# Optimization experiments

Measured on AMD Instinct MI355X. Metric: run time of the kernel, lower is better.

## Reference

```python
import jax, jax.numpy as jnp
import numpy as np

B, C, H, W = 512, 1, 128, 128
RS, WS = 12, 12
L, HID, T = 128, 512, 16


def setup_inputs() -> dict:
    key = jax.random.key(0)
    ks = jax.random.split(key, 24)

    def u(k, shape, fan):
        return jax.random.uniform(k, shape, jnp.float32, -1.0, 1.0) / np.sqrt(fan)

    enc_in = 2 * RS * RS + HID  # 800
    inp = {
        "x": jax.random.uniform(ks[0], (B, C, H, W), jnp.float32),
        "eps": jax.random.normal(ks[1], (T, B, L), jnp.float32),
        "glimpses": T,
        "canvas_init": jnp.zeros((C, H, W), jnp.float32),
        "h_dec_init": jnp.zeros((HID,), jnp.float32),
        "h_enc_init": jnp.zeros((HID,), jnp.float32),
        "W_ih_enc": u(ks[2], (4 * HID, enc_in), enc_in),
        "b_ih_enc": u(ks[3], (4 * HID,), enc_in),
        "W_hh_enc": u(ks[4], (4 * HID, HID), HID),
        "b_hh_enc": u(ks[5], (4 * HID,), HID),
        "W_ih_dec": u(ks[6], (4 * HID, L), L),
        "b_ih_dec": u(ks[7], (4 * HID,), L),
        "W_hh_dec": u(ks[8], (4 * HID, HID), HID),
        "b_hh_dec": u(ks[9], (4 * HID,), HID),
        "W_samp": u(ks[10], (2 * L, HID), HID),
        "b_samp": u(ks[11], (2 * L,), HID),
        "W_rattn": u(ks[12], (5, HID), HID),
        "b_rattn": u(ks[13], (5,), HID),
        "W_wattn": u(ks[14], (5, HID), HID),
        "b_wattn": u(ks[15], (5,), HID),
        "W_writer": u(ks[16], (WS * WS, HID), HID),
        "b_writer": u(ks[17], (WS * WS,), HID),
    }
    return inp


def _lstm_cell(x, h, c, Wih, bih, Whh, bhh):
    gates = x @ Wih.T + bih + h @ Whh.T + bhh
    i, f, g, o = jnp.split(gates, 4, axis=-1)
    c_new = jax.nn.sigmoid(f) * c + jax.nn.sigmoid(i) * jnp.tanh(g)
    h_new = jax.nn.sigmoid(o) * jnp.tanh(c_new)
    return h_new, c_new


def _filter_bank(gx, gy, variance, stride, size):
    # gx, gy, variance, stride: [B,1]
    offsets = (jnp.arange(size, dtype=jnp.float32) + 0.5 - size / 2) * stride  # [B,size]
    mu_x = (gx + offsets)[..., None]  # [B,size,1]
    mu_y = (gy + offsets)[..., None]
    var = variance[:, :, None]  # [B,1,1]
    a = jnp.arange(W, dtype=jnp.float32)
    b = jnp.arange(H, dtype=jnp.float32)
    Fx = jnp.exp(-((a - mu_x) ** 2) / (2 * var))  # [B,size,W]
    Fy = jnp.exp(-((b - mu_y) ** 2) / (2 * var))  # [B,size,H]
    Fx = Fx / jnp.maximum(Fx.sum(axis=2, keepdims=True), 1e-8)
    Fy = Fy / jnp.maximum(Fy.sum(axis=2, keepdims=True), 1e-8)
    return Fx, Fy


def _attn_window(h_state, Wattn, battn, size):
    res = h_state @ Wattn.T + battn  # [B,5]
    gx_, gy_, log_var, log_delta, log_inten = [res[:, i:i + 1] for i in range(5)]
    gx = (W + 1) * (gx_ + 1) / 2
    gy = (H + 1) * (gy_ + 1) / 2
    stride = (max(H, W) - 1) * jnp.exp(log_delta) / (size - 1)
    Fx, Fy = _filter_bank(gx, gy, jnp.exp(log_var), stride, size)
    return Fx, Fy, jnp.exp(log_inten)


def _read(x, x_error, h_dec, W_rattn, b_rattn):
    Fx, Fy, inten = _attn_window(h_dec, W_rattn, b_rattn, RS)
    FxT = jnp.swapaxes(Fx, -1, -2)[:, None]  # [B,1,W,RS]
    Fy = Fy[:, None]  # [B,1,RS,H]
    glimpse = jnp.concatenate((Fy @ x @ FxT, Fy @ x_error @ FxT), axis=1)  # [B,2C,RS,RS]
    return inten[:, :, None, None] * glimpse


def _write(h_dec, W_writer, b_writer, W_wattn, b_wattn):
    w = (h_dec @ W_writer.T + b_writer).reshape(-1, C, WS, WS)
    Fx, Fy, inten = _attn_window(h_dec, W_wattn, b_wattn, WS)
    FyT = jnp.swapaxes(Fy, -1, -2)[:, None]  # [B,1,H,WS]
    Fx = Fx[:, None]  # [B,1,WS,W]
    return (FyT @ w @ Fx) / inten[:, :, None, None]  # [B,C,H,W]


def reference(x, eps, glimpses, canvas_init, h_dec_init, h_enc_init,
              W_ih_enc, b_ih_enc, W_hh_enc, b_hh_enc,
              W_ih_dec, b_ih_dec, W_hh_dec, b_hh_dec,
              W_samp, b_samp, W_rattn, b_rattn, W_wattn, b_wattn,
              W_writer, b_writer):
    batch = x.shape[0]
    canvas0 = jnp.broadcast_to(canvas_init, (batch, C, H, W))
    h_dec0 = jnp.broadcast_to(h_dec_init, (batch, HID))
    h_enc0 = jnp.broadcast_to(h_enc_init, (batch, HID))
    c0 = jnp.zeros((batch, HID), x.dtype)

    def step(carry, eps_t):
        canvas, h_enc, c_enc, h_dec, c_dec = carry
        x_error = x - jax.nn.sigmoid(canvas)
        r = _read(x, x_error, h_dec, W_rattn, b_rattn).reshape(batch, -1)
        enc_in = jnp.concatenate((r, h_dec), axis=1)
        h_enc, c_enc = _lstm_cell(enc_in, h_enc, c_enc, W_ih_enc, b_ih_enc, W_hh_enc, b_hh_enc)
        s = h_enc @ W_samp.T + b_samp
        mu, log_var = s[:, :L], s[:, L:]
        z = mu + jnp.exp(log_var * 0.5) * eps_t
        h_dec, c_dec = _lstm_cell(z, h_dec, c_dec, W_ih_dec, b_ih_dec, W_hh_dec, b_hh_dec)
        canvas = canvas + _write(h_dec, W_writer, b_writer, W_wattn, b_wattn)
        return (canvas, h_enc, c_enc, h_dec, c_dec), (mu, log_var)

    (canvas, _, _, _, _), (mus, log_vars) = jax.lax.scan(
        step, (canvas0, h_enc0, c0, h_dec0, c0), eps[:glimpses])
    # mus/log_vars: [T,B,L] -> [B,T,L] to match torch.stack(mu, dim=1)
    return jax.nn.sigmoid(canvas), jnp.swapaxes(mus, 0, 1), jnp.swapaxes(log_vars, 0, 1)
```

## Files before the change

kernel.cpp:

```cpp
#include <hip/hip_runtime.h>
#include <hip/hip_bf16.h>
#include <math.h>

#define BATCH 512
#define HID 512
#define LAT 128
#define TSTEPS 16
#define IMG 16384
#define ENC_IN 800
#define GATES 2048

#define SEC_E 1344
#define SEC_D 640

typedef __attribute__((ext_vector_type(8))) short short8;
typedef __attribute__((ext_vector_type(4))) float f32x4;

__device__ __forceinline__ void gload16(const void* g, void* l) {
    __builtin_amdgcn_global_load_lds((const __attribute__((address_space(1))) unsigned int*)g,
                                     (__attribute__((address_space(3))) unsigned int*)l, 16, 0, 0);
}

__device__ __forceinline__ void bsplit(float v, unsigned short& hi, unsigned short& lo) {
    unsigned u = __float_as_uint(v);
    unsigned uh = (u + (0x7FFFu + ((u >> 16) & 1u))) & 0xFFFF0000u;
    hi = (unsigned short)(uh >> 16);
    float r = v - __uint_as_float(uh);
    unsigned ur = __float_as_uint(r);
    unsigned ul = (ur + (0x7FFFu + ((ur >> 16) & 1u))) & 0xFFFF0000u;
    lo = (unsigned short)(ul >> 16);
}

__global__ __launch_bounds__(256) void init_canvas(float* __restrict__ canvas,
                                                   const float* __restrict__ ci) {
    int idx = blockIdx.x * 256 + threadIdx.x;
    canvas[idx] = ci[idx & (IMG - 1)];
}

__global__ __launch_bounds__(256) void init_state(float* __restrict__ he, float* __restrict__ ce,
                                                  float* __restrict__ hd, float* __restrict__ cd,
                                                  const float* __restrict__ hei,
                                                  const float* __restrict__ hdi,
                                                  unsigned short* __restrict__ A_enc,
                                                  unsigned short* __restrict__ A_dec) {
    int idx = blockIdx.x * 256 + threadIdx.x;
    int b = idx >> 9, u = idx & 511;
    float ve = hei[u], vd = hdi[u];
    he[idx] = ve;
    hd[idx] = vd;
    ce[idx] = 0.f;
    cd[idx] = 0.f;
    unsigned short hi, lo;
    bsplit(ve, hi, lo);
    size_t be = (size_t)b * 2 * SEC_E;
    A_enc[be + 800 + u] = hi;
    A_enc[be + SEC_E + 800 + u] = lo;
    bsplit(vd, hi, lo);
    size_t bd = (size_t)b * 2 * SEC_D;
    A_dec[bd + 128 + u] = hi;
    A_dec[bd + SEC_D + 128 + u] = lo;
}

__global__ __launch_bounds__(256) void sigmoid_final(float* __restrict__ c) {
    int idx = blockIdx.x * 256 + threadIdx.x;
    c[idx] = 1.f / (1.f + expf(-c[idx]));
}

__global__ __launch_bounds__(256) void prep_wsplit(const float* __restrict__ W1, int K1,
                                                   const float* __restrict__ W2, int K2,
                                                   unsigned short* __restrict__ out, int SEC) {
    int kk = blockIdx.x * 256 + threadIdx.x;
    int n = blockIdx.y;
    if (kk >= SEC) return;
    float v = 0.f;
    if (kk < K1) v = W1[(size_t)n * K1 + kk];
    else if (kk < K1 + K2) v = W2[(size_t)n * K2 + (kk - K1)];
    unsigned short hi, lo;
    bsplit(v, hi, lo);
    size_t base = (size_t)n * 2 * SEC;
    out[base + kk] = hi;
    out[base + SEC + kk] = lo;
}

__global__ __launch_bounds__(256) void gemm_bf16x3(const unsigned short* __restrict__ Au,
                                                   const unsigned short* __restrict__ Wu,
                                                   float* __restrict__ C, int SEC,
                                                   int ktb0, int kte0, int ktb1, int kte1) {
    __shared__ __align__(16) char lds[2][16384];
    const __bf16* A = (const __bf16*)Au;
    const __bf16* Wt = (const __bf16*)Wu;
    const int ld = 2 * SEC;
    const int tid = threadIdx.x;
    const int z = blockIdx.z;
    const int bm = blockIdx.x * 64;
    const int bn = blockIdx.y * 64;
    const int ktb = z ? ktb1 : ktb0;
    const int kte = z ? kte1 : kte0;

    const int row0 = tid >> 3, c0 = tid & 7;
    const size_t ga0 = (size_t)(bm + row0) * ld + (size_t)((c0 ^ (row0 & 7)) * 8);
    const size_t ga1 = ga0 + (size_t)32 * ld;
    const size_t gb0 = (size_t)(bn + row0) * ld + (size_t)((c0 ^ (row0 & 7)) * 8);
    const size_t gb1 = gb0 + (size_t)32 * ld;
    const int lA0 = tid * 16, lA1 = (tid + 256) * 16;
    const int lB0 = 8192 + tid * 16, lB1 = 8192 + (tid + 256) * 16;

    const int lane = tid & 63, wv = tid >> 6;
    const int rA = wv * 16 + (lane & 15);
    const int chnk = (lane >> 4) ^ (lane & 7);
    const int byteA = rA * 128 + chnk * 16;
    const int byteB = 8192 + (lane & 15) * 128 + chnk * 16;

    f32x4 acc[4];
#pragma unroll
    for (int j = 0; j < 4; ++j) acc[j] = (f32x4){0.f, 0.f, 0.f, 0.f};

    auto STAGE = [&](int buf, int kt) {
        const int kw = kt * 64;
        const int ka = (kw >= SEC) ? (kw - SEC) : kw;
        const int kb = (kw >= 2 * SEC) ? (kw - 2 * SEC) : kw;
        const __bf16* a = A + ka;
        const __bf16* w = Wt + kb;
        char* l = &lds[buf][0];
        gload16(a + ga0, l + lA0);
        gload16(a + ga1, l + lA1);
        gload16(w + gb0, l + lB0);
        gload16(w + gb1, l + lB1);
    };

    STAGE(0, ktb);
    asm volatile("s_waitcnt vmcnt(0)" ::: "memory");
    __syncthreads();
    int buf = 0;
    for (int kt = ktb; kt < kte; ++kt) {
        if (kt + 1 < kte) STAGE(buf ^ 1, kt + 1);
        const char* base = &lds[buf][0];
        short8 a0 = *(const short8*)(base + byteA);
        short8 a1 = *(const short8*)(base + (byteA ^ 64));
#pragma unroll
        for (int j = 0; j < 4; ++j) {
            short8 b0 = *(const short8*)(base + (byteB + j * 2048));
            short8 b1 = *(const short8*)(base + ((byteB + j * 2048) ^ 64));
            acc[j] = __builtin_amdgcn_mfma_f32_16x16x32_bf16(a0, b0, acc[j], 0, 0, 0);
            acc[j] = __builtin_amdgcn_mfma_f32_16x16x32_bf16(a1, b1, acc[j], 0, 0, 0);
        }
        asm volatile("s_waitcnt vmcnt(0)" ::: "memory");
        __syncthreads();
        buf ^= 1;
    }
    float* Cz = C + (size_t)z * BATCH * GATES;
    const int crow = bm + wv * 16 + (lane >> 4) * 4;
    const int ccol = bn + (lane & 15);
#pragma unroll
    for (int j = 0; j < 4; ++j)
#pragma unroll
        for (int r = 0; r < 4; ++r)
            Cz[(size_t)(crow + r) * GATES + ccol + j * 16] = acc[j][r];
}

__global__ __launch_bounds__(256) void read_glimpse_fused(const float* __restrict__ x,
                                                          const float* __restrict__ canvas,
                                                          const float* __restrict__ h_dec,
                                                          const float* __restrict__ Wa,
                                                          const float* __restrict__ ba,
                                                          unsigned short* __restrict__ A_enc) {
    const int b = blockIdx.x, t = threadIdx.x;
    __shared__ float red[5][256];
    __shared__ float par[5];
    __shared__ float fx[12][132], fy[12][132];
    __shared__ float dnx[12], dny[12];
    __shared__ float pbuf[4][12][128];
    __shared__ float tm[12][132], te[12][132];
    const float* hb = h_dec + (size_t)b * HID;
#pragma unroll
    for (int j = 0; j < 5; ++j)
        red[j][t] = hb[t] * Wa[j * HID + t] + hb[t + 256] * Wa[j * HID + t + 256];
    __syncthreads();
    for (int o = 128; o > 0; o >>= 1) {
        if (t < o) {
#pragma unroll
            for (int j = 0; j < 5; ++j) red[j][t] += red[j][t + o];
        }
        __syncthreads();
    }
    if (t < 5) par[t] = red[t][0] + ba[t];
    __syncthreads();
    const float gx = 129.f * (par[0] + 1.f) * 0.5f;
    const float gy = 129.f * (par[1] + 1.f) * 0.5f;
    const float var = expf(par[2]);
    const float strd = 127.f * expf(par[3]) / 11.f;
    const float iv = expf(par[4]);
    const int col = t & 127;
    const float a = (float)col;
    if (t < 128) {
#pragma unroll
        for (int i = 0; i < 12; ++i) {
            float d = a - (gx + ((float)i + 0.5f - 6.f) * strd);
            fx[i][col] = expf(-(d * d) / (2.f * var));
        }
    } else {
#pragma unroll
        for (int i = 0; i < 12; ++i) {
            float d = a - (gy + ((float)i + 0.5f - 6.f) * strd);
            fy[i][col] = expf(-(d * d) / (2.f * var));
        }
    }
    __syncthreads();
    if (t < 12) {
        float s = 0.f;
        for (int k = 0; k < 128; ++k) s += fx[t][k];
        dnx[t] = fmaxf(s, 1e-8f);
    } else if (t >= 128 && t < 140) {
        float s = 0.f;
        for (int k = 0; k < 128; ++k) s += fy[t - 128][k];
        dny[t - 128] = fmaxf(s, 1e-8f);
    }
    __syncthreads();
    if (t < 128) {
#pragma unroll
        for (int i = 0; i < 12; ++i) fx[i][col] /= dnx[i];
    } else {
#pragma unroll
        for (int i = 0; i < 12; ++i) fy[i][col] /= dny[i];
    }
    __syncthreads();
    const int g = t >> 6, p = t & 63, c2 = p * 2;
    float2 acc2[12] = {}, acce2[12] = {};
    const float* xb = x + (size_t)b * IMG;
    const float* cb = canvas + (size_t)b * IMG;
    for (int hh = g * 32; hh < g * 32 + 32; ++hh) {
        float2 xv = *(const float2*)(xb + hh * 128 + c2);
        float2 cv = *(const float2*)(cb + hh * 128 + c2);
        float2 xe;
        xe.x = xv.x - 1.f / (1.f + expf(-cv.x));
        xe.y = xv.y - 1.f / (1.f + expf(-cv.y));
#pragma unroll
        for (int i = 0; i < 12; ++i) {
            float f = fy[i][hh];
            acc2[i].x += f * xv.x;
            acc2[i].y += f * xv.y;
            acce2[i].x += f * xe.x;
            acce2[i].y += f * xe.y;
        }
    }
#pragma unroll
    for (int i = 0; i < 12; ++i) *(float2*)(&pbuf[g][i][c2]) = acc2[i];
    __syncthreads();
    for (int it = t; it < 1536; it += 256) {
        int ii = it >> 7, cc = it & 127;
        tm[ii][cc] = pbuf[0][ii][cc] + pbuf[1][ii][cc] + pbuf[2][ii][cc] + pbuf[3][ii][cc];
    }
    __syncthreads();
#pragma unroll
    for (int i = 0; i < 12; ++i) *(float2*)(&pbuf[g][i][c2]) = acce2[i];
    __syncthreads();
    for (int it = t; it < 1536; it += 256) {
        int ii = it >> 7, cc = it & 127;
        te[ii][cc] = pbuf[0][ii][cc] + pbuf[1][ii][cc] + pbuf[2][ii][cc] + pbuf[3][ii][cc];
    }
    __syncthreads();
    unsigned short hi, lo;
    unsigned short* rb = A_enc + (size_t)b * 2 * SEC_E;
    for (int o = t; o < 288; o += 256) {
        int ch = (o >= 144) ? 1 : 0;
        int rem = o - ch * 144;
        int ii = rem / 12, jj = rem - ii * 12;
        const float* src = ch ? te[ii] : tm[ii];
        float s = 0.f;
        for (int w2 = 0; w2 < 128; ++w2) s += src[w2] * fx[jj][w2];
        bsplit(iv * s, hi, lo);
        rb[o] = hi;
        rb[SEC_E + o] = lo;
    }
    for (int u = t; u < HID; u += 256) {
        bsplit(hb[u], hi, lo);
        rb[288 + u] = hi;
        rb[SEC_E + 288 + u] = lo;
    }
    if (t < 32) {
        rb[1312 + t] = 0;
        rb[SEC_E + 1312 + t] = 0;
    }
}

template <int TM, int TN>
__global__ __launch_bounds__(256) void gemm_slab(const float* __restrict__ A0,
                                                 const float* __restrict__ W0,
                                                 const float* __restrict__ bias0, int ld0, int K0,
                                                 const float* __restrict__ A1,
                                                 const float* __restrict__ W1,
                                                 const float* __restrict__ bias1, int ld1, int K1,
                                                 float* __restrict__ C, int M, int N) {
    constexpr int BM = 16 * TM, BN = 16 * TN, BK = 16;
    __shared__ float As[BK][BM + 4];
    __shared__ float Ws[BK][BN + 4];
    const int z = blockIdx.z;
    const float* A = z ? A1 : A0;
    const float* Wm = z ? W1 : W0;
    const float* bs = z ? bias1 : bias0;
    const int ld = z ? ld1 : ld0;
    const int K = z ? K1 : K0;
    const int tid = threadIdx.x;
    const int tx = tid & 15, ty = tid >> 4;
    const int bm = blockIdx.x * BM, bn = blockIdx.y * BN;
    float acc[TM][TN] = {};
    for (int k0 = 0; k0 < K; k0 += BK) {
        __syncthreads();
        for (int i = tid; i < BM * 4; i += 256) {
            int row = i >> 2, c4 = i & 3;
            const float4 v = *(const float4*)(A + (size_t)(bm + row) * ld + k0 + c4 * 4);
            As[c4 * 4 + 0][row] = v.x;
            As[c4 * 4 + 1][row] = v.y;
            As[c4 * 4 + 2][row] = v.z;
            As[c4 * 4 + 3][row] = v.w;
        }
        for (int i = tid; i < BN * 4; i += 256) {
            int row = i >> 2, c4 = i & 3;
            int wr = bn + row;
            float4 v = make_float4(0.f, 0.f, 0.f, 0.f);
            if (wr < N) v = *(const float4*)(Wm + (size_t)wr * ld + k0 + c4 * 4);
            Ws[c4 * 4 + 0][row] = v.x;
            Ws[c4 * 4 + 1][row] = v.y;
            Ws[c4 * 4 + 2][row] = v.z;
            Ws[c4 * 4 + 3][row] = v.w;
        }
        __syncthreads();
#pragma unroll
        for (int c = 0; c < BK; ++c) {
            float a[TM], w[TN];
#pragma unroll
            for (int i = 0; i < TM; ++i) a[i] = As[c][ty * TM + i];
#pragma unroll
            for (int j = 0; j < TN; ++j) w[j] = Ws[c][tx * TN + j];
#pragma unroll
            for (int i = 0; i < TM; ++i)
#pragma unroll
                for (int j = 0; j < TN; ++j) acc[i][j] += a[i] * w[j];
        }
    }
    float* Cz = C + (size_t)z * M * N;
#pragma unroll
    for (int i = 0; i < TM; ++i) {
        const int rr = bm + ty * TM + i;
#pragma unroll
        for (int j = 0; j < TN; ++j) {
            const int cc = bn + tx * TN + j;
            if (cc < N) Cz[(size_t)rr * N + cc] = acc[i][j] + (bs ? bs[cc] : 0.f);
        }
    }
}

__global__ __launch_bounds__(256) void lstm_pw(const float* __restrict__ g0,
                                               const float* __restrict__ g1,
                                               const float* __restrict__ bih,
                                               const float* __restrict__ bhh,
                                               float* __restrict__ h, float* __restrict__ c,
                                               unsigned short* __restrict__ split_out,
                                               int soff, int SEC2) {
    int idx = blockIdx.x * 256 + threadIdx.x;
    int b = idx >> 9, u = idx & 511;
    size_t base = (size_t)b * GATES;
    float gi = g0[base + u] + g1[base + u] + bih[u] + bhh[u];
    float gf = g0[base + 512 + u] + g1[base + 512 + u] + bih[512 + u] + bhh[512 + u];
    float gg = g0[base + 1024 + u] + g1[base + 1024 + u] + bih[1024 + u] + bhh[1024 + u];
    float go = g0[base + 1536 + u] + g1[base + 1536 + u] + bih[1536 + u] + bhh[1536 + u];
    float si = 1.f / (1.f + expf(-gi));
    float sf = 1.f / (1.f + expf(-gf));
    float so = 1.f / (1.f + expf(-go));
    float cn = sf * c[idx] + si * tanhf(gg);
    c[idx] = cn;
    float hn = so * tanhf(cn);
    h[idx] = hn;
    unsigned short hi, lo;
    bsplit(hn, hi, lo);
    size_t sb = (size_t)b * 2 * SEC2;
    split_out[sb + soff + u] = hi;
    split_out[sb + SEC2 + soff + u] = lo;
}

__global__ __launch_bounds__(256) void z_kernel(const float* __restrict__ s,
                                                const float* __restrict__ eps_t,
                                                unsigned short* __restrict__ A_dec,
                                                float* __restrict__ mu_out,
                                                float* __restrict__ lv_out, int t) {
    int idx = blockIdx.x * 256 + threadIdx.x;
    int b = idx >> 7, l = idx & 127;
    int i0 = b * 256 + l;
    float mu = s[i0] + s[131072 + i0];
    float lv = s[i0 + 128] + s[131072 + i0 + 128];
    float zv = mu + expf(0.5f * lv) * eps_t[idx];
    unsigned short hi, lo;
    bsplit(zv, hi, lo);
    size_t bd = (size_t)b * 2 * SEC_D;
    A_dec[bd + l] = hi;
    A_dec[bd + SEC_D + l] = lo;
    size_t o = (size_t)b * (TSTEPS * LAT) + t * LAT + l;
    mu_out[o] = mu;
    lv_out[o] = lv;
}

__global__ __launch_bounds__(256) void write_canvas_fused(float* __restrict__ canvas,
                                                          const float* __restrict__ w0,
                                                          const float* __restrict__ w1,
                                                          const float* __restrict__ h_dec,
                                                          const float* __restrict__ Wa,
                                                          const float* __restrict__ ba) {
    const int b = blockIdx.x, t = threadIdx.x;
    __shared__ float red[5][256];
    __shared__ float par[5];
    __shared__ float fx[12][132], fyl[12][132];
    __shared__ float dnx[12], dny[12];
    __shared__ float wl[12][12], tl[128][13];
    const float* hb = h_dec + (size_t)b * HID;
#pragma unroll
    for (int j = 0; j < 5; ++j)
        red[j][t] = hb[t] * Wa[j * HID + t] + hb[t + 256] * Wa[j * HID + t + 256];
    __syncthreads();
    for (int o = 128; o > 0; o >>= 1) {
        if (t < o) {
#pragma unroll
            for (int j = 0; j < 5; ++j) red[j][t] += red[j][t + o];
        }
        __syncthreads();
    }
    if (t < 5) par[t] = red[t][0] + ba[t];
    __syncthreads();
    const float gx = 129.f * (par[0] + 1.f) * 0.5f;
    const float gy = 129.f * (par[1] + 1.f) * 0.5f;
    const float var = expf(par[2]);
    const float strd = 127.f * expf(par[3]) / 11.f;
    const float riv = 1.f / expf(par[4]);
    const int col = t & 127;
    const float a = (float)col;
    if (t < 128) {
#pragma unroll
        for (int i = 0; i < 12; ++i) {
            float d = a - (gx + ((float)i + 0.5f - 6.f) * strd);
            fx[i][col] = expf(-(d * d) / (2.f * var));
        }
    } else {
#pragma unroll
        for (int i = 0; i < 12; ++i) {
            float d = a - (gy + ((float)i + 0.5f - 6.f) * strd);
            fyl[i][col] = expf(-(d * d) / (2.f * var));
        }
    }
    for (int i = t; i < 144; i += 256) wl[i / 12][i % 12] = w0[(size_t)b * 144 + i] + w1[(size_t)b * 144 + i];
    __syncthreads();
    if (t < 12) {
        float s = 0.f;
        for (int k = 0; k < 128; ++k) s += fx[t][k];
        dnx[t] = fmaxf(s, 1e-8f);
    } else if (t >= 128 && t < 140) {
        float s = 0.f;
        for (int k = 0; k < 128; ++k) s += fyl[t - 128][k];
        dny[t - 128] = fmaxf(s, 1e-8f);
    }
    __syncthreads();
    if (t < 128) {
#pragma unroll
        for (int i = 0; i < 12; ++i) fx[i][col] /= dnx[i];
    } else {
#pragma unroll
        for (int i = 0; i < 12; ++i) fyl[i][col] /= dny[i];
    }
    __syncthreads();
    if (t < 128) {
        float tj[12] = {};
#pragma unroll
        for (int i = 0; i < 12; ++i) {
            float f = fyl[i][t];
#pragma unroll
            for (int j = 0; j < 12; ++j) tj[j] += f * wl[i][j];
        }
#pragma unroll
        for (int j = 0; j < 12; ++j) tl[t][j] = tj[j];
    }
    __syncthreads();
    const int g = t >> 6, p = t & 63, c2 = p * 2;
    float* cb = canvas + (size_t)b * IMG;
    for (int hh = g * 32; hh < g * 32 + 32; ++hh) {
        float sx = 0.f, sy = 0.f;
#pragma unroll
        for (int j = 0; j < 12; ++j) {
            float tv = tl[hh][j];
            sx += tv * fx[j][c2];
            sy += tv * fx[j][c2 + 1];
        }
        float2 cv = *(float2*)(cb + hh * 128 + c2);
        cv.x += sx * riv;
        cv.y += sy * riv;
        *(float2*)(cb + hh * 128 + c2) = cv;
    }
}

extern "C" void kernel_launch(void* const* d_in, const int* in_sizes, int n_in,
                              void* d_out, int out_size, void* d_ws, size_t ws_size,
                              hipStream_t stream) {
    const float* x = (const float*)d_in[0];
    const float* eps = (const float*)d_in[1];
    const float* canvas_init = (const float*)d_in[3];
    const float* h_dec_init = (const float*)d_in[4];
    const float* h_enc_init = (const float*)d_in[5];
    const float* W_ih_enc = (const float*)d_in[6];
    const float* b_ih_enc = (const float*)d_in[7];
    const float* W_hh_enc = (const float*)d_in[8];
    const float* b_hh_enc = (const float*)d_in[9];
    const float* W_ih_dec = (const float*)d_in[10];
    const float* b_ih_dec = (const float*)d_in[11];
    const float* W_hh_dec = (const float*)d_in[12];
    const float* b_hh_dec = (const float*)d_in[13];
    const float* W_samp = (const float*)d_in[14];
    const float* b_samp = (const float*)d_in[15];
    const float* W_rattn = (const float*)d_in[16];
    const float* b_rattn = (const float*)d_in[17];
    const float* W_wattn = (const float*)d_in[18];
    const float* b_wattn = (const float*)d_in[19];
    const float* W_writer = (const float*)d_in[20];
    const float* b_writer = (const float*)d_in[21];

    float* out = (float*)d_out;
    float* canvas = out;
    float* out_mu = out + (size_t)BATCH * IMG;
    float* out_lv = out_mu + (size_t)BATCH * TSTEPS * LAT;

    float* ws = (float*)d_ws;
    size_t off = 0;
    auto alloc = [&](size_t n) { float* p = ws + off; off += n; return p; };
    float* h_enc = alloc((size_t)BATCH * HID);
    float* c_enc = alloc((size_t)BATCH * HID);
    float* h_dec = alloc((size_t)BATCH * HID);
    float* c_dec = alloc((size_t)BATCH * HID);
    float* gates = alloc((size_t)2 * BATCH * GATES);
    float* sbuf = alloc((size_t)2 * BATCH * 256);
    float* wbuf = alloc((size_t)2 * BATCH * 144);
    unsigned short* A_enc = (unsigned short*)alloc((size_t)BATCH * SEC_E);
    unsigned short* A_dec = (unsigned short*)alloc((size_t)BATCH * SEC_D);
    unsigned short* Ws_enc = (unsigned short*)alloc((size_t)GATES * SEC_E);
    unsigned short* Ws_dec = (unsigned short*)alloc((size_t)GATES * SEC_D);

    init_canvas<<<BATCH * IMG / 256, 256, 0, stream>>>(canvas, canvas_init);
    init_state<<<BATCH * HID / 256, 256, 0, stream>>>(h_enc, c_enc, h_dec, c_dec,
                                                      h_enc_init, h_dec_init, A_enc, A_dec);
    prep_wsplit<<<dim3((SEC_E + 255) / 256, GATES), 256, 0, stream>>>(W_ih_enc, ENC_IN, W_hh_enc, HID, Ws_enc, SEC_E);
    prep_wsplit<<<dim3((SEC_D + 255) / 256, GATES), 256, 0, stream>>>(W_ih_dec, LAT, W_hh_dec, HID, Ws_dec, SEC_D);

    const int ktE = 3 * SEC_E / 64;
    const int ktD = 3 * SEC_D / 64;

    for (int t = 0; t < TSTEPS; ++t) {
        read_glimpse_fused<<<BATCH, 256, 0, stream>>>(x, canvas, h_dec, W_rattn, b_rattn, A_enc);
        gemm_bf16x3<<<dim3(BATCH / 64, GATES / 64, 2), 256, 0, stream>>>(
            A_enc, Ws_enc, gates, SEC_E, 0, 32, 32, ktE);
        lstm_pw<<<BATCH * HID / 256, 256, 0, stream>>>(gates, gates + (size_t)BATCH * GATES,
                                                       b_ih_enc, b_hh_enc, h_enc, c_enc,
                                                       A_enc, 800, SEC_E);
        gemm_slab<4, 1><<<dim3(8, 16, 2), 256, 0, stream>>>(
            h_enc, W_samp, b_samp, HID, 256,
            h_enc + 256, W_samp + 256, nullptr, HID, 256, sbuf, BATCH, 256);
        z_kernel<<<BATCH * LAT / 256, 256, 0, stream>>>(sbuf, eps + (size_t)t * BATCH * LAT,
                                                        A_dec, out_mu, out_lv, t);
        gemm_bf16x3<<<dim3(BATCH / 64, GATES / 64, 2), 256, 0, stream>>>(
            A_dec, Ws_dec, gates, SEC_D, 0, 15, 15, ktD);
        lstm_pw<<<BATCH * HID / 256, 256, 0, stream>>>(gates, gates + (size_t)BATCH * GATES,
                                                       b_ih_dec, b_hh_dec, h_dec, c_dec,
                                                       A_dec, 128, SEC_D);
        gemm_slab<4, 1><<<dim3(8, 9, 2), 256, 0, stream>>>(
            h_dec, W_writer, b_writer, HID, 256,
            h_dec + 256, W_writer + 256, nullptr, HID, 256, wbuf, BATCH, 144);
        write_canvas_fused<<<BATCH, 256, 0, stream>>>(canvas, wbuf, wbuf + (size_t)BATCH * 144,
                                                      h_dec, W_wattn, b_wattn);
    }
    sigmoid_final<<<BATCH * IMG / 256, 256, 0, stream>>>(canvas);
}
```

Baseline: 2.080 ms.

## Fuse writer GEMM into write_canvas kernel and widen glimpse kernels to 512 threads

The separate gemm_slab launch that computed the 144-wide writer patch is removed. Each write_canvas block now computes its own patch from h_dec and W_writer with wave-level shuffle reductions. Both read and write glimpse kernels move from 256 to 512 threads per block, halving rows per thread and spreading filter-bank construction across all threads. This saves one launch and a global round trip per step, at the cost of each block re-reading the full writer weight matrix (about 295KB) and using more shared memory per block.

Measured after the change: 1.962 ms. 1.06x faster.

```diff
diff --git a/kernel.cpp b/kernel.cpp
--- a/kernel.cpp
+++ b/kernel.cpp
@@ -158,77 +158,73 @@
             Cz[(size_t)(crow + r) * GATES + ccol + j * 16] = acc[j][r];
 }
 
-__global__ __launch_bounds__(256) void read_glimpse_fused(const float* __restrict__ x,
-                                                          const float* __restrict__ canvas,
-                                                          const float* __restrict__ h_dec,
-                                                          const float* __restrict__ Wa,
-                                                          const float* __restrict__ ba,
-                                                          unsigned short* __restrict__ A_enc) {
+__global__ __launch_bounds__(512, 4) void read_glimpse_fused(const float* __restrict__ x,
+                                                             const float* __restrict__ canvas,
+                                                             const float* __restrict__ h_dec,
+                                                             const float* __restrict__ Wa,
+                                                             const float* __restrict__ ba,
+                                                             unsigned short* __restrict__ A_enc) {
     const int b = blockIdx.x, t = threadIdx.x;
-    __shared__ float red[5][256];
     __shared__ float par[5];
     __shared__ float fx[12][132], fy[12][132];
-    __shared__ float dnx[12], dny[12];
-    __shared__ float pbuf[4][12][128];
+    __shared__ float dn[24];
     __shared__ float tm[12][132], te[12][132];
+    __shared__ __align__(16) float pbuf[8][12][128];
+    float* red = &pbuf[0][0][0];
     const float* hb = h_dec + (size_t)b * HID;
 #pragma unroll
-    for (int j = 0; j < 5; ++j)
-        red[j][t] = hb[t] * Wa[j * HID + t] + hb[t + 256] * Wa[j * HID + t + 256];
-    __syncthreads();
-    for (int o = 128; o > 0; o >>= 1) {
+    for (int j = 0; j < 5; ++j) red[j * 512 + t] = hb[t] * Wa[j * HID + t];
+    __syncthreads();
+    for (int o = 256; o > 0; o >>= 1) {
         if (t < o) {
 #pragma unroll
-            for (int j = 0; j < 5; ++j) red[j][t] += red[j][t + o];
+            for (int j = 0; j < 5; ++j) red[j * 512 + t] += red[j * 512 + t + o];
         }
         __syncthreads();
     }
-    if (t < 5) par[t] = red[t][0] + ba[t];
+    if (t < 5) par[t] = red[t * 512] + ba[t];
     __syncthreads();
     const float gx = 129.f * (par[0] + 1.f) * 0.5f;
     const float gy = 129.f * (par[1] + 1.f) * 0.5f;
     const float var = expf(par[2]);
     const float strd = 127.f * expf(par[3]) / 11.f;
     const float iv = expf(par[4]);
-    const int col = t & 127;
-    const float a = (float)col;
-    if (t < 128) {
-#pragma unroll
-        for (int i = 0; i < 12; ++i) {
-            float d = a - (gx + ((float)i + 0.5f - 6.f) * strd);
-            fx[i][col] = expf(-(d * d) / (2.f * var));
-        }
-    } else {
-#pragma unroll
-        for (int i = 0; i < 12; ++i) {
-            float d = a - (gy + ((float)i + 0.5f - 6.f) * strd);
-            fy[i][col] = expf(-(d * d) / (2.f * var));
-        }
-    }
-    __syncthreads();
-    if (t < 12) {
+#pragma unroll
+    for (int rep = 0; rep < 6; ++rep) {
+        int e = t + rep * 512;
+        int mat = e / 1536;
+        int rr = (e - mat * 1536) >> 7;
+        int cc = e & 127;
+        float ctr = (mat ? gy : gx) + ((float)rr + 0.5f - 6.f) * strd;
+        float d = (float)cc - ctr;
+        float v = expf(-(d * d) / (2.f * var));
+        float (*dst)[132] = mat ? fy : fx;
+        dst[rr][cc] = v;
+    }
+    __syncthreads();
+    if (t < 24) {
+        const float (*src)[132] = (t < 12) ? fx : fy;
+        int rr = (t < 12) ? t : t - 12;
         float s = 0.f;
-        for (int k = 0; k < 128; ++k) s += fx[t][k];
-        dnx[t] = fmaxf(s, 1e-8f);
-    } else if (t >= 128 && t < 140) {
-        float s = 0.f;
-        for (int k = 0; k < 128; ++k) s += fy[t - 128][k];
-        dny[t - 128] = fmaxf(s, 1e-8f);
-    }
-    __syncthreads();
-    if (t < 128) {
-#pragma unroll
-        for (int i = 0; i < 12; ++i) fx[i][col] /= dnx[i];
-    } else {
-#pragma unroll
-        for (int i = 0; i < 12; ++i) fy[i][col] /= dny[i];
-    }
-    __syncthreads();
-    const int g = t >> 6, p = t & 63, c2 = p * 2;
-    float2 acc2[12] = {}, acce2[12] = {};
+        for (int k = 0; k < 128; ++k) s += src[rr][k];
+        dn[t] = fmaxf(s, 1e-8f);
+    }
+    __syncthreads();
+#pragma unroll
+    for (int rep = 0; rep < 6; ++rep) {
+        int e = t + rep * 512;
+        int mat = e / 1536;
+        int rr = (e - mat * 1536) >> 7;
+        int cc = e & 127;
+        float (*dst)[132] = mat ? fy : fx;
+        dst[rr][cc] /= dn[mat * 12 + rr];
+    }
+    __syncthreads();
+    const int g = t >> 6, l = t & 63, c2 = l * 2;
+    float2 am[12] = {}, ae[12] = {};
     const float* xb = x + (size_t)b * IMG;
     const float* cb = canvas + (size_t)b * IMG;
-    for (int hh = g * 32; hh < g * 32 + 32; ++hh) {
+    for (int hh = g * 16; hh < g * 16 + 16; ++hh) {
         float2 xv = *(const float2*)(xb + hh * 128 + c2);
         float2 cv = *(const float2*)(cb + hh * 128 + c2);
         float2 xe;
@@ -237,46 +233,50 @@
 #pragma unroll
         for (int i = 0; i < 12; ++i) {
             float f = fy[i][hh];
-            acc2[i].x += f * xv.x;
-            acc2[i].y += f * xv.y;
-            acce2[i].x += f * xe.x;
-            acce2[i].y += f * xe.y;
-        }
-    }
-#pragma unroll
-    for (int i = 0; i < 12; ++i) *(float2*)(&pbuf[g][i][c2]) = acc2[i];
-    __syncthreads();
-    for (int it = t; it < 1536; it += 256) {
+            am[i].x += f * xv.x;
+            am[i].y += f * xv.y;
+            ae[i].x += f * xe.x;
+            ae[i].y += f * xe.y;
+        }
+    }
+#pragma unroll
+    for (int i = 0; i < 12; ++i) *(float2*)(&pbuf[g][i][c2]) = am[i];
+    __syncthreads();
+    for (int it = t; it < 1536; it += 512) {
         int ii = it >> 7, cc = it & 127;
-        tm[ii][cc] = pbuf[0][ii][cc] + pbuf[1][ii][cc] + pbuf[2][ii][cc] + pbuf[3][ii][cc];
-    }
-    __syncthreads();
-#pragma unroll
-    for (int i = 0; i < 12; ++i) *(float2*)(&pbuf[g][i][c2]) = acce2[i];
-    __syncthreads();
-    for (int it = t; it < 1536; it += 256) {
+        float s = 0.f;
+#pragma unroll
+        for (int k = 0; k < 8; ++k) s += pbuf[k][ii][cc];
+        tm[ii][cc] = s;
+    }
+    __syncthreads();
+#pragma unroll
+    for (int i = 0; i < 12; ++i) *(float2*)(&pbuf[g][i][c2]) = ae[i];
+    __syncthreads();
+    for (int it = t; it < 1536; it += 512) {
         int ii = it >> 7, cc = it & 127;
-        te[ii][cc] = pbuf[0][ii][cc] + pbuf[1][ii][cc] + pbuf[2][ii][cc] + pbuf[3][ii][cc];
+        float s = 0.f;
+#pragma unroll
+        for (int k = 0; k < 8; ++k) s += pbuf[k][ii][cc];
+        te[ii][cc] = s;
     }
     __syncthreads();
     unsigned short hi, lo;
     unsigned short* rb = A_enc + (size_t)b * 2 * SEC_E;
-    for (int o = t; o < 288; o += 256) {
-        int ch = (o >= 144) ? 1 : 0;
-        int rem = o - ch * 144;
+    if (t < 288) {
+        int ch = (t >= 144) ? 1 : 0;
+        int rem = t - ch * 144;
         int ii = rem / 12, jj = rem - ii * 12;
         const float* src = ch ? te[ii] : tm[ii];
         float s = 0.f;
         for (int w2 = 0; w2 < 128; ++w2) s += src[w2] * fx[jj][w2];
         bsplit(iv * s, hi, lo);
-        rb[o] = hi;
-        rb[SEC_E + o] = lo;
-    }
-    for (int u = t; u < HID; u += 256) {
-        bsplit(hb[u], hi, lo);
-        rb[288 + u] = hi;
-        rb[SEC_E + 288 + u] = lo;
-    }
+        rb[t] = hi;
+        rb[SEC_E + t] = lo;
+    }
+    bsplit(hb[t], hi, lo);
+    rb[288 + t] = hi;
+    rb[SEC_E + 288 + t] = lo;
     if (t < 32) {
         rb[1312 + t] = 0;
         rb[SEC_E + 1312 + t] = 0;
@@ -399,24 +399,27 @@
     lv_out[o] = lv;
 }
 
-__global__ __launch_bounds__(256) void write_canvas_fused(float* __restrict__ canvas,
-                                                          const float* __restrict__ w0,
-                                                          const float* __restrict__ w1,
-                                                          const float* __restrict__ h_dec,
-                                                          const float* __restrict__ Wa,
-                                                          const float* __restrict__ ba) {
+__global__ __launch_bounds__(512, 4) void write_canvas_fused(float* __restrict__ canvas,
+                                                             const float* __restrict__ h_dec,
+                                                             const float* __restrict__ Wr,
+                                                             const float* __restrict__ bwr,
+                                                             const float* __restrict__ Wa,
+                                                             const float* __restrict__ ba) {
     const int b = blockIdx.x, t = threadIdx.x;
-    __shared__ float red[5][256];
     __shared__ float par[5];
+    __shared__ float hl[512];
+    __shared__ float red[5][512];
     __shared__ float fx[12][132], fyl[12][132];
-    __shared__ float dnx[12], dny[12];
-    __shared__ float wl[12][12], tl[128][13];
+    __shared__ float dn[24];
+    __shared__ float wl[144];
+    __shared__ float tl[128][13];
     const float* hb = h_dec + (size_t)b * HID;
-#pragma unroll
-    for (int j = 0; j < 5; ++j)
-        red[j][t] = hb[t] * Wa[j * HID + t] + hb[t + 256] * Wa[j * HID + t + 256];
-    __syncthreads();
-    for (int o = 128; o > 0; o >>= 1) {
+    hl[t] = hb[t];
+    __syncthreads();
+#pragma unroll
+    for (int j = 0; j < 5; ++j) red[j][t] = hl[t] * Wa[j * HID + t];
+    __syncthreads();
+    for (int o = 256; o > 0; o >>= 1) {
         if (t < o) {
 #pragma unroll
             for (int j = 0; j < 5; ++j) red[j][t] += red[j][t + o];
@@ -430,39 +433,48 @@
     const float var = expf(par[2]);
     const float strd = 127.f * expf(par[3]) / 11.f;
     const float riv = 1.f / expf(par[4]);
-    const int col = t & 127;
-    const float a = (float)col;
-    if (t < 128) {
-#pragma unroll
-        for (int i = 0; i < 12; ++i) {
-            float d = a - (gx + ((float)i + 0.5f - 6.f) * strd);
-            fx[i][col] = expf(-(d * d) / (2.f * var));
-        }
-    } else {
-#pragma unroll
-        for (int i = 0; i < 12; ++i) {
-            float d = a - (gy + ((float)i + 0.5f - 6.f) * strd);
-            fyl[i][col] = expf(-(d * d) / (2.f * var));
-        }
-    }
-    for (int i = t; i < 144; i += 256) wl[i / 12][i % 12] = w0[(size_t)b * 144 + i] + w1[(size_t)b * 144 + i];
-    __syncthreads();
-    if (t < 12) {
+#pragma unroll
+    for (int rep = 0; rep < 6; ++rep) {
+        int e = t + rep * 512;
+        int mat = e / 1536;
+        int rr = (e - mat * 1536) >> 7;
+        int cc = e & 127;
+        float ctr = (mat ? gy : gx) + ((float)rr + 0.5f - 6.f) * strd;
+        float d = (float)cc - ctr;
+        float v = expf(-(d * d) / (2.f * var));
+        float (*dst)[132] = mat ? fyl : fx;
+        dst[rr][cc] = v;
+    }
+    {
+        const int wv = t >> 6, l = t & 63;
+#pragma unroll
+        for (int oi = 0; oi < 18; ++oi) {
+            int o = wv * 18 + oi;
+            float p = 0.f;
+#pragma unroll
+            for (int j = 0; j < 8; ++j) p += hl[l + 64 * j] * Wr[(size_t)o * 512 + l + 64 * j];
+#pragma unroll
+            for (int m = 32; m; m >>= 1) p += __shfl_xor(p, m, 64);
+            if (l == 0) wl[o] = p + bwr[o];
+        }
+    }
+    __syncthreads();
+    if (t < 24) {
+        const float (*src)[132] = (t < 12) ? fx : fyl;
+        int rr = (t < 12) ? t : t - 12;
         float s = 0.f;
-        for (int k = 0; k < 128; ++k) s += fx[t][k];
-        dnx[t] = fmaxf(s, 1e-8f);
-    } else if (t >= 128 && t < 140) {
-        float s = 0.f;
-        for (int k = 0; k < 128; ++k) s += fyl[t - 128][k];
-        dny[t - 128] = fmaxf(s, 1e-8f);
-    }
-    __syncthreads();
-    if (t < 128) {
-#pragma unroll
-        for (int i = 0; i < 12; ++i) fx[i][col] /= dnx[i];
-    } else {
-#pragma unroll
-        for (int i = 0; i < 12; ++i) fyl[i][col] /= dny[i];
+        for (int k = 0; k < 128; ++k) s += src[rr][k];
+        dn[t] = fmaxf(s, 1e-8f);
+    }
+    __syncthreads();
+#pragma unroll
+    for (int rep = 0; rep < 6; ++rep) {
+        int e = t + rep * 512;
+        int mat = e / 1536;
+        int rr = (e - mat * 1536) >> 7;
+        int cc = e & 127;
+        float (*dst)[132] = mat ? fyl : fx;
+        dst[rr][cc] /= dn[mat * 12 + rr];
     }
     __syncthreads();
     if (t < 128) {
@@ -471,15 +483,15 @@
         for (int i = 0; i < 12; ++i) {
             float f = fyl[i][t];
 #pragma unroll
-            for (int j = 0; j < 12; ++j) tj[j] += f * wl[i][j];
+            for (int j = 0; j < 12; ++j) tj[j] += f * wl[i * 12 + j];
         }
 #pragma unroll
         for (int j = 0; j < 12; ++j) tl[t][j] = tj[j];
     }
     __syncthreads();
-    const int g = t >> 6, p = t & 63, c2 = p * 2;
+    const int g = t >> 6, l = t & 63, c2 = l * 2;
     float* cb = canvas + (size_t)b * IMG;
-    for (int hh = g * 32; hh < g * 32 + 32; ++hh) {
+    for (int hh = g * 16; hh < g * 16 + 16; ++hh) {
         float sx = 0.f, sy = 0.f;
 #pragma unroll
         for (int j = 0; j < 12; ++j) {
@@ -533,7 +545,6 @@
     float* c_dec = alloc((size_t)BATCH * HID);
     float* gates = alloc((size_t)2 * BATCH * GATES);
     float* sbuf = alloc((size_t)2 * BATCH * 256);
-    float* wbuf = alloc((size_t)2 * BATCH * 144);
     unsigned short* A_enc = (unsigned short*)alloc((size_t)BATCH * SEC_E);
     unsigned short* A_dec = (unsigned short*)alloc((size_t)BATCH * SEC_D);
     unsigned short* Ws_enc = (unsigned short*)alloc((size_t)GATES * SEC_E);
@@ -549,7 +560,7 @@
     const int ktD = 3 * SEC_D / 64;
 
     for (int t = 0; t < TSTEPS; ++t) {
-        read_glimpse_fused<<<BATCH, 256, 0, stream>>>(x, canvas, h_dec, W_rattn, b_rattn, A_enc);
+        read_glimpse_fused<<<BATCH, 512, 0, stream>>>(x, canvas, h_dec, W_rattn, b_rattn, A_enc);
         gemm_bf16x3<<<dim3(BATCH / 64, GATES / 64, 2), 256, 0, stream>>>(
             A_enc, Ws_enc, gates, SEC_E, 0, 32, 32, ktE);
         lstm_pw<<<BATCH * HID / 256, 256, 0, stream>>>(gates, gates + (size_t)BATCH * GATES,
@@ -565,11 +576,8 @@
         lstm_pw<<<BATCH * HID / 256, 256, 0, stream>>>(gates, gates + (size_t)BATCH * GATES,
                                                        b_ih_dec, b_hh_dec, h_dec, c_dec,
                                                        A_dec, 128, SEC_D);
-        gemm_slab<4, 1><<<dim3(8, 9, 2), 256, 0, stream>>>(
-            h_dec, W_writer, b_writer, HID, 256,
-            h_dec + 256, W_writer + 256, nullptr, HID, 256, wbuf, BATCH, 144);
-        write_canvas_fused<<<BATCH, 256, 0, stream>>>(canvas, wbuf, wbuf + (size_t)BATCH * 144,
-                                                      h_dec, W_wattn, b_wattn);
+        write_canvas_fused<<<BATCH, 512, 0, stream>>>(canvas, h_dec, W_writer, b_writer,
+                                                      W_wattn, b_wattn);
     }
     sigmoid_final<<<BATCH * IMG / 256, 256, 0, stream>>>(canvas);
 }
```
